# Performance work log

Measured on AMD Instinct MI355X. Metric: run time of the kernel, lower is better.

Reference implementation:

```python
import jax, jax.numpy as jnp
import numpy as np

D_MODEL = 1024
NUM_HEADS = 16
ENERGY_SCALE = 0.1
LN_EPS = 1e-5


def layernorm(x, gamma, beta):
    mu = jnp.mean(x, axis=-1, keepdims=True)
    var = jnp.var(x, axis=-1, keepdims=True)
    return (x - mu) * jax.lax.rsqrt(var + LN_EPS) * gamma + beta


def setup_inputs() -> dict:
    key = jax.random.key(0)
    ks = jax.random.split(key, 8)
    B, L, D = 2, 2048, D_MODEL
    s = 0.02
    return {
        "x": jax.random.normal(ks[0], (B, L, D), dtype=jnp.float32),
        "wq": jax.random.normal(ks[1], (D, D), dtype=jnp.float32) * s,
        "wk": jax.random.normal(ks[2], (D, D), dtype=jnp.float32) * s,
        "wv": jax.random.normal(ks[3], (D, D), dtype=jnp.float32) * s,
        "wo_w": jax.random.normal(ks[4], (D, D), dtype=jnp.float32) * s,
        "wo_b": jnp.zeros((D,), dtype=jnp.float32),
        "ep_w": jax.random.normal(ks[5], (D, D), dtype=jnp.float32) * s,
        "ep_b": jnp.zeros((D,), dtype=jnp.float32),
        "en_g": jnp.ones((D,), dtype=jnp.float32),
        "en_b": jnp.zeros((D,), dtype=jnp.float32),
        "ln_g": jnp.ones((D,), dtype=jnp.float32),
        "ln_b": jnp.zeros((D,), dtype=jnp.float32),
    }


def reference(x, wq, wk, wv, wo_w, wo_b, ep_w, ep_b, en_g, en_b, ln_g, ln_b):
    B, L, D = x.shape
    H, dk = NUM_HEADS, D // NUM_HEADS
    # Linear projections (torch convention: y = x @ W^T), split heads -> [B,H,L,dk]
    q = (x @ wq.T).reshape(B, L, H, dk).transpose(0, 2, 1, 3)
    k = (x @ wk.T).reshape(B, L, H, dk).transpose(0, 2, 1, 3)
    v = (x @ wv.T).reshape(B, L, H, dk).transpose(0, 2, 1, 3)
    scores = jnp.einsum("bhld,bhmd->bhlm", q, k) / jnp.sqrt(jnp.float32(dk))
    # Energy bias: ef @ ef^T as a proper GEMM (same math as the broadcast-mul-sum)
    ef = layernorm(x @ ep_w.T + ep_b, en_g, en_b)
    energy_bias = jnp.einsum("bld,bmd->blm", ef, ef)  # [B,L,L]
    scores = scores + ENERGY_SCALE * energy_bias[:, None, :, :]
    attn = jax.nn.softmax(scores, axis=-1)  # dropout is identity in eval mode
    ctx = jnp.einsum("bhlm,bhmd->bhld", attn, v)
    ctx = ctx.transpose(0, 2, 1, 3).reshape(B, L, D)
    out = ctx @ wo_w.T + wo_b
    return layernorm(out + x, ln_g, ln_b), attn
```

## Files before the change

kernel.cpp:

```cpp
#include <hip/hip_runtime.h>
#include <math.h>

#define D_MODEL 1024
#define NUM_HEADS 16
#define DK 64
#define L_SEQ 2048
#define BATCH 2
#define LN_EPS 1e-5f
#define ENERGY_SCALE 0.1f

typedef __attribute__((ext_vector_type(8))) short short8;
typedef __attribute__((ext_vector_type(4))) float f32x4;

__device__ __forceinline__ float waveReduceSum(float v) {
#pragma unroll
    for (int off = 32; off > 0; off >>= 1) v += __shfl_xor(v, off, 64);
    return v;
}

__device__ __forceinline__ unsigned short f2bf(float f) {
    unsigned int u = __float_as_uint(f);
    u += 0x7fff + ((u >> 16) & 1);
    return (unsigned short)(u >> 16);
}

__global__ __launch_bounds__(256) void cvt6(
    const float* s0, const float* s1, const float* s2,
    const float* s3, const float* s4, const float* s5,
    unsigned short* d0, unsigned short* d1, unsigned short* d2,
    unsigned short* d3, unsigned short* d4, unsigned short* d5,
    long long n0, long long n1, long long n2, long long n3, long long n4, long long n5)
{
    const float* s; unsigned short* d; long long n;
    switch (blockIdx.y) {
        case 0: s = s0; d = d0; n = n0; break;
        case 1: s = s1; d = d1; n = n1; break;
        case 2: s = s2; d = d2; n = n2; break;
        case 3: s = s3; d = d3; n = n3; break;
        case 4: s = s4; d = d4; n = n4; break;
        default: s = s5; d = d5; n = n5; break;
    }
    long long i = ((long long)blockIdx.x * 256 + threadIdx.x) * 4;
    if (i >= n) return;
    float4 v = *(const float4*)(s + i);
    ushort4 o;
    o.x = f2bf(v.x); o.y = f2bf(v.y); o.z = f2bf(v.z); o.w = f2bf(v.w);
    *(ushort4*)(d + i) = o;
}

__global__ __launch_bounds__(256) void gemm_bf16(
    const unsigned short* __restrict__ A, const unsigned short* __restrict__ B,
    const float* __restrict__ bias, float* __restrict__ Cf, unsigned short* __restrict__ Ch,
    int N, int K, long long sA, long long sB, long long sC)
{
    A += (long long)blockIdx.z * sA;
    B += (long long)blockIdx.z * sB;
    __shared__ unsigned short As[128 * 72];
    __shared__ unsigned short Bs[128 * 72];
    const int tid = threadIdx.x;
    const int lane = tid & 63, w = tid >> 6;
    const int quad = lane >> 4, col = lane & 15;
    const int wm = w & 1, wn = w >> 1;
    const int row0 = blockIdx.y * 128, col0 = blockIdx.x * 128;

    f32x4 acc[4][4];
#pragma unroll
    for (int mt = 0; mt < 4; mt++)
#pragma unroll
        for (int nt = 0; nt < 4; nt++) acc[mt][nt] = (f32x4){0.f, 0.f, 0.f, 0.f};

    for (int k0 = 0; k0 < K; k0 += 64) {
        __syncthreads();
#pragma unroll
        for (int p = 0; p < 4; p++) {
            int u = tid + p * 256;
            int r = u >> 3;
            int c = (u & 7) * 8;
            *(uint4*)(As + r * 72 + c) = *(const uint4*)(A + (long long)(row0 + r) * K + k0 + c);
            *(uint4*)(Bs + r * 72 + c) = *(const uint4*)(B + (long long)(col0 + r) * K + k0 + c);
        }
        __syncthreads();
#pragma unroll
        for (int kc = 0; kc < 2; kc++) {
            short8 af[4], bfr[4];
#pragma unroll
            for (int mt = 0; mt < 4; mt++)
                af[mt] = *(const short8*)(As + (wm * 64 + mt * 16 + col) * 72 + quad * 8 + kc * 32);
#pragma unroll
            for (int nt = 0; nt < 4; nt++)
                bfr[nt] = *(const short8*)(Bs + (wn * 64 + nt * 16 + col) * 72 + quad * 8 + kc * 32);
#pragma unroll
            for (int mt = 0; mt < 4; mt++)
#pragma unroll
                for (int nt = 0; nt < 4; nt++)
                    acc[mt][nt] = __builtin_amdgcn_mfma_f32_16x16x32_bf16(af[mt], bfr[nt], acc[mt][nt], 0, 0, 0);
        }
    }

#pragma unroll
    for (int mt = 0; mt < 4; mt++)
#pragma unroll
        for (int nt = 0; nt < 4; nt++)
#pragma unroll
            for (int reg = 0; reg < 4; reg++) {
                long long row = row0 + wm * 64 + mt * 16 + quad * 4 + reg;
                int c = col0 + wn * 64 + nt * 16 + col;
                float v = acc[mt][nt][reg];
                if (bias) v += bias[c];
                if (Cf) Cf[blockIdx.z * sC + row * N + c] = v;
                else    Ch[blockIdx.z * sC + row * N + c] = f2bf(v);
            }
}

__global__ __launch_bounds__(256) void proj_gemm(
    const unsigned short* __restrict__ Xh,
    const unsigned short* __restrict__ wqh, const unsigned short* __restrict__ wkh,
    const unsigned short* __restrict__ wvh, const unsigned short* __restrict__ eph,
    const float* __restrict__ ep_b,
    unsigned short* __restrict__ Qh, unsigned short* __restrict__ Kh,
    unsigned short* __restrict__ Vf, float* __restrict__ EP)
{
    const unsigned short* B;
    switch (blockIdx.z) {
        case 0: B = wqh; break;
        case 1: B = wkh; break;
        case 2: B = wvh; break;
        default: B = eph; break;
    }
    __shared__ unsigned short As[128 * 72];
    __shared__ unsigned short Bs[128 * 72];
    const int tid = threadIdx.x;
    const int lane = tid & 63, w = tid >> 6;
    const int quad = lane >> 4, col = lane & 15;
    const int wm = w & 1, wn = w >> 1;
    const int row0 = blockIdx.y * 128, col0 = blockIdx.x * 128;
    const int K = D_MODEL, N = D_MODEL;

    f32x4 acc[4][4];
#pragma unroll
    for (int mt = 0; mt < 4; mt++)
#pragma unroll
        for (int nt = 0; nt < 4; nt++) acc[mt][nt] = (f32x4){0.f, 0.f, 0.f, 0.f};

    for (int k0 = 0; k0 < K; k0 += 64) {
        __syncthreads();
#pragma unroll
        for (int p = 0; p < 4; p++) {
            int u = tid + p * 256;
            int r = u >> 3;
            int c = (u & 7) * 8;
            *(uint4*)(As + r * 72 + c) = *(const uint4*)(Xh + (long long)(row0 + r) * K + k0 + c);
            *(uint4*)(Bs + r * 72 + c) = *(const uint4*)(B + (long long)(col0 + r) * K + k0 + c);
        }
        __syncthreads();
#pragma unroll
        for (int kc = 0; kc < 2; kc++) {
            short8 af[4], bfr[4];
#pragma unroll
            for (int mt = 0; mt < 4; mt++)
                af[mt] = *(const short8*)(As + (wm * 64 + mt * 16 + col) * 72 + quad * 8 + kc * 32);
#pragma unroll
            for (int nt = 0; nt < 4; nt++)
                bfr[nt] = *(const short8*)(Bs + (wn * 64 + nt * 16 + col) * 72 + quad * 8 + kc * 32);
#pragma unroll
            for (int mt = 0; mt < 4; mt++)
#pragma unroll
                for (int nt = 0; nt < 4; nt++)
                    acc[mt][nt] = __builtin_amdgcn_mfma_f32_16x16x32_bf16(af[mt], bfr[nt], acc[mt][nt], 0, 0, 0);
        }
    }

    unsigned short* Hout = (blockIdx.z == 0) ? Qh : (blockIdx.z == 1) ? Kh : Vf;
#pragma unroll
    for (int mt = 0; mt < 4; mt++)
#pragma unroll
        for (int nt = 0; nt < 4; nt++)
#pragma unroll
            for (int reg = 0; reg < 4; reg++) {
                long long row = row0 + wm * 64 + mt * 16 + quad * 4 + reg;
                int c = col0 + wn * 64 + nt * 16 + col;
                float v = acc[mt][nt][reg];
                if (blockIdx.z == 3) EP[row * N + c] = v + ep_b[c];
                else                 Hout[row * N + c] = f2bf(v);
            }
}

__global__ __launch_bounds__(256) void ln_rows(
    const float* __restrict__ in, const float* __restrict__ res,
    const float* __restrict__ g, const float* __restrict__ bta,
    float* __restrict__ outf, unsigned short* __restrict__ outh)
{
    const long long row = blockIdx.x;
    const float* ip = in + row * D_MODEL;
    const float* rp = res ? res + row * D_MODEL : nullptr;
    const int tid = threadIdx.x;
    float vals[4];
    float s = 0.f, ss = 0.f;
#pragma unroll
    for (int j = 0; j < 4; j++) {
        int idx = tid + j * 256;
        float v = ip[idx];
        if (rp) v += rp[idx];
        vals[j] = v; s += v; ss += v * v;
    }
    __shared__ float sred[4], ssred[4];
    s = waveReduceSum(s); ss = waveReduceSum(ss);
    int wave = tid >> 6, lane = tid & 63;
    if (lane == 0) { sred[wave] = s; ssred[wave] = ss; }
    __syncthreads();
    float ts = sred[0] + sred[1] + sred[2] + sred[3];
    float tss = ssred[0] + ssred[1] + ssred[2] + ssred[3];
    float mu = ts * (1.f / D_MODEL);
    float var = tss * (1.f / D_MODEL) - mu * mu;
    float rs = rsqrtf(var + LN_EPS);
#pragma unroll
    for (int j = 0; j < 4; j++) {
        int idx = tid + j * 256;
        float o = (vals[j] - mu) * rs * g[idx] + bta[idx];
        if (outf) outf[row * D_MODEL + idx] = o;
        else      outh[row * D_MODEL + idx] = f2bf(o);
    }
}

__global__ __launch_bounds__(256) void transpose_v(
    const unsigned short* __restrict__ V, unsigned short* __restrict__ Vt)
{
    const int m0 = blockIdx.x * 64, h = blockIdx.y, b = blockIdx.z;
    __shared__ unsigned int t[64][65];
    const int tid = threadIdx.x;
    {
        int r = tid >> 4, c4 = (tid & 15) * 4;
#pragma unroll
        for (int i = 0; i < 4; i++) {
            int row = r + i * 16;
            ushort4 v = *(const ushort4*)(V + ((long long)b * L_SEQ + m0 + row) * D_MODEL + h * DK + c4);
            t[row][c4] = v.x; t[row][c4 + 1] = v.y; t[row][c4 + 2] = v.z; t[row][c4 + 3] = v.w;
        }
    }
    __syncthreads();
    const int lane = tid & 63, wv = tid >> 6;
#pragma unroll
    for (int i = 0; i < 16; i++) {
        int d = wv * 16 + i;
        Vt[(((long long)(b * NUM_HEADS + h)) * DK + d) * L_SEQ + m0 + lane] = (unsigned short)t[lane][d];
    }
}

__global__ __launch_bounds__(256) void attn_mfma(
    const unsigned short* __restrict__ Qh, const unsigned short* __restrict__ Kh,
    const unsigned short* __restrict__ Vt, const float* __restrict__ EB,
    float* __restrict__ attn_out, unsigned short* __restrict__ CTXh)
{
    __shared__ unsigned short smem[5 * 64 * 72];
    unsigned short* K0 = smem;
    unsigned short* K1 = smem + 4608;
    unsigned short* V0 = smem + 2 * 4608;
    unsigned short* V1 = smem + 3 * 4608;
    unsigned short* Ps = smem + 4 * 4608;

    const int tid = threadIdx.x;
    const int lane = tid & 63, w = tid >> 6;
    const int quad = lane >> 4, col = lane & 15;
    const int l0 = blockIdx.x * 64;
    const int h = blockIdx.y, b = blockIdx.z;

    short8 aq[2];
    {
        const unsigned short* qrow = Qh + ((long long)b * L_SEQ + l0 + w * 16 + col) * D_MODEL + h * DK;
        aq[0] = *(const short8*)(qrow + quad * 8);
        aq[1] = *(const short8*)(qrow + 32 + quad * 8);
    }

    const float* ebp = EB + ((long long)b * L_SEQ + l0 + w * 16 + quad * 4) * L_SEQ + col;
    const unsigned short* kbase = Kh + ((long long)b * L_SEQ) * D_MODEL + h * DK;
    const unsigned short* vbase = Vt + ((long long)(b * NUM_HEADS + h)) * DK * L_SEQ;

    const int sr = tid >> 2, sc0 = (tid & 3) * 16;

    float rowM[4] = {-1e30f, -1e30f, -1e30f, -1e30f};
    float rowS[4] = {0.f, 0.f, 0.f, 0.f};
    float ebc[4][4];

    {
        *(uint4*)(K0 + sr * 72 + sc0)     = *(const uint4*)(kbase + (long long)sr * D_MODEL + sc0);
        *(uint4*)(K0 + sr * 72 + sc0 + 8) = *(const uint4*)(kbase + (long long)sr * D_MODEL + sc0 + 8);
#pragma unroll
        for (int nt = 0; nt < 4; nt++)
#pragma unroll
            for (int reg = 0; reg < 4; reg++)
                ebc[nt][reg] = ebp[(long long)reg * L_SEQ + nt * 16];
    }
    __syncthreads();

    for (int t = 0; t < 32; t++) {
        unsigned short* cur = (t & 1) ? K1 : K0;
        unsigned short* nxt = (t & 1) ? K0 : K1;
        uint4 ka, kb;
        float ebn[4][4];
        if (t < 31) {
            const int m1 = (t + 1) * 64;
            ka = *(const uint4*)(kbase + (long long)(m1 + sr) * D_MODEL + sc0);
            kb = *(const uint4*)(kbase + (long long)(m1 + sr) * D_MODEL + sc0 + 8);
#pragma unroll
            for (int nt = 0; nt < 4; nt++)
#pragma unroll
                for (int reg = 0; reg < 4; reg++)
                    ebn[nt][reg] = ebp[(long long)reg * L_SEQ + m1 + nt * 16];
        }

        f32x4 acc[4];
#pragma unroll
        for (int nt = 0; nt < 4; nt++) acc[nt] = (f32x4){0.f, 0.f, 0.f, 0.f};
#pragma unroll
        for (int nt = 0; nt < 4; nt++)
#pragma unroll
            for (int kc = 0; kc < 2; kc++) {
                short8 bk = *(const short8*)(cur + (nt * 16 + col) * 72 + quad * 8 + kc * 32);
                acc[nt] = __builtin_amdgcn_mfma_f32_16x16x32_bf16(aq[kc], bk, acc[nt], 0, 0, 0);
            }

        float sv[4][4];
#pragma unroll
        for (int nt = 0; nt < 4; nt++)
#pragma unroll
            for (int reg = 0; reg < 4; reg++)
                sv[nt][reg] = acc[nt][reg] * 0.125f + ENERGY_SCALE * ebc[nt][reg];

#pragma unroll
        for (int reg = 0; reg < 4; reg++) {
            float tm = fmaxf(fmaxf(sv[0][reg], sv[1][reg]), fmaxf(sv[2][reg], sv[3][reg]));
#pragma unroll
            for (int off = 8; off > 0; off >>= 1) tm = fmaxf(tm, __shfl_xor(tm, off, 64));
            float nm = fmaxf(rowM[reg], tm);
            float tsum = __expf(sv[0][reg] - nm) + __expf(sv[1][reg] - nm) +
                         __expf(sv[2][reg] - nm) + __expf(sv[3][reg] - nm);
#pragma unroll
            for (int off = 8; off > 0; off >>= 1) tsum += __shfl_xor(tsum, off, 64);
            rowS[reg] = rowS[reg] * __expf(rowM[reg] - nm) + tsum;
            rowM[reg] = nm;
        }

        if (t < 31) {
            *(uint4*)(nxt + sr * 72 + sc0)     = ka;
            *(uint4*)(nxt + sr * 72 + sc0 + 8) = kb;
        }
        __syncthreads();
        if (t < 31) {
#pragma unroll
            for (int nt = 0; nt < 4; nt++)
#pragma unroll
                for (int reg = 0; reg < 4; reg++)
                    ebc[nt][reg] = ebn[nt][reg];
        }
    }

    float invS[4];
#pragma unroll
    for (int reg = 0; reg < 4; reg++) invS[reg] = 1.f / rowS[reg];

    f32x4 ctx[4];
#pragma unroll
    for (int nt = 0; nt < 4; nt++) ctx[nt] = (f32x4){0.f, 0.f, 0.f, 0.f};

    unsigned short* Psw = Ps + w * 16 * 72;
    float* aob = attn_out + (((long long)(b * NUM_HEADS + h)) * L_SEQ + l0 + w * 16 + quad * 4) * L_SEQ + col;

    {
        *(uint4*)(K0 + sr * 72 + sc0)     = *(const uint4*)(kbase + (long long)sr * D_MODEL + sc0);
        *(uint4*)(K0 + sr * 72 + sc0 + 8) = *(const uint4*)(kbase + (long long)sr * D_MODEL + sc0 + 8);
        *(uint4*)(V0 + sr * 72 + sc0)     = *(const uint4*)(vbase + (long long)sr * L_SEQ + sc0);
        *(uint4*)(V0 + sr * 72 + sc0 + 8) = *(const uint4*)(vbase + (long long)sr * L_SEQ + sc0 + 8);
#pragma unroll
        for (int nt = 0; nt < 4; nt++)
#pragma unroll
            for (int reg = 0; reg < 4; reg++)
                ebc[nt][reg] = ebp[(long long)reg * L_SEQ + nt * 16];
    }
    __syncthreads();

    for (int t = 0; t < 32; t++) {
        const int m0 = t * 64;
        unsigned short* curK = (t & 1) ? K1 : K0;
        unsigned short* nxtK = (t & 1) ? K0 : K1;
        unsigned short* curV = (t & 1) ? V1 : V0;
        unsigned short* nxtV = (t & 1) ? V0 : V1;
        uint4 ka, kb, va, vb;
        float ebn[4][4];
        if (t < 31) {
            const int m1 = m0 + 64;
            ka = *(const uint4*)(kbase + (long long)(m1 + sr) * D_MODEL + sc0);
            kb = *(const uint4*)(kbase + (long long)(m1 + sr) * D_MODEL + sc0 + 8);
            va = *(const uint4*)(vbase + (long long)sr * L_SEQ + m1 + sc0);
            vb = *(const uint4*)(vbase + (long long)sr * L_SEQ + m1 + sc0 + 8);
#pragma unroll
            for (int nt = 0; nt < 4; nt++)
#pragma unroll
                for (int reg = 0; reg < 4; reg++)
                    ebn[nt][reg] = ebp[(long long)reg * L_SEQ + m1 + nt * 16];
        }

        f32x4 acc[4];
#pragma unroll
        for (int nt = 0; nt < 4; nt++) acc[nt] = (f32x4){0.f, 0.f, 0.f, 0.f};
#pragma unroll
        for (int nt = 0; nt < 4; nt++)
#pragma unroll
            for (int kc = 0; kc < 2; kc++) {
                short8 bk = *(const short8*)(curK + (nt * 16 + col) * 72 + quad * 8 + kc * 32);
                acc[nt] = __builtin_amdgcn_mfma_f32_16x16x32_bf16(aq[kc], bk, acc[nt], 0, 0, 0);
            }

        float pv[4][4];
#pragma unroll
        for (int nt = 0; nt < 4; nt++)
#pragma unroll
            for (int reg = 0; reg < 4; reg++) {
                float s = acc[nt][reg] * 0.125f + ENERGY_SCALE * ebc[nt][reg];
                float p = __expf(s - rowM[reg]) * invS[reg];
                pv[nt][reg] = p;
                Psw[(quad * 4 + reg) * 72 + nt * 16 + col] = f2bf(p);
            }

        short8 ap[2];
#pragma unroll
        for (int kc = 0; kc < 2; kc++)
            ap[kc] = *(const short8*)(Psw + col * 72 + quad * 8 + kc * 32);
#pragma unroll
        for (int nt = 0; nt < 4; nt++)
#pragma unroll
            for (int kc = 0; kc < 2; kc++) {
                short8 bv = *(const short8*)(curV + (nt * 16 + col) * 72 + quad * 8 + kc * 32);
                ctx[nt] = __builtin_amdgcn_mfma_f32_16x16x32_bf16(ap[kc], bv, ctx[nt], 0, 0, 0);
            }

#pragma unroll
        for (int nt = 0; nt < 4; nt++)
#pragma unroll
            for (int reg = 0; reg < 4; reg++)
                aob[(long long)reg * L_SEQ + m0 + nt * 16] = pv[nt][reg];

        if (t < 31) {
            *(uint4*)(nxtK + sr * 72 + sc0)     = ka;
            *(uint4*)(nxtK + sr * 72 + sc0 + 8) = kb;
            *(uint4*)(nxtV + sr * 72 + sc0)     = va;
            *(uint4*)(nxtV + sr * 72 + sc0 + 8) = vb;
        }
        __syncthreads();
        if (t < 31) {
#pragma unroll
            for (int nt = 0; nt < 4; nt++)
#pragma unroll
                for (int reg = 0; reg < 4; reg++)
                    ebc[nt][reg] = ebn[nt][reg];
        }
    }

#pragma unroll
    for (int nt = 0; nt < 4; nt++)
#pragma unroll
        for (int reg = 0; reg < 4; reg++)
            CTXh[((long long)b * L_SEQ + l0 + w * 16 + quad * 4 + reg) * D_MODEL + h * DK + nt * 16 + col] =
                f2bf(ctx[nt][reg]);
}

extern "C" void kernel_launch(void* const* d_in, const int* in_sizes, int n_in,
                              void* d_out, int out_size, void* d_ws, size_t ws_size,
                              hipStream_t stream) {
    const float* x    = (const float*)d_in[0];
    const float* wq   = (const float*)d_in[1];
    const float* wk   = (const float*)d_in[2];
    const float* wv   = (const float*)d_in[3];
    const float* wo_w = (const float*)d_in[4];
    const float* wo_b = (const float*)d_in[5];
    const float* ep_w = (const float*)d_in[6];
    const float* ep_b = (const float*)d_in[7];
    const float* en_g = (const float*)d_in[8];
    const float* en_b = (const float*)d_in[9];
    const float* ln_g = (const float*)d_in[10];
    const float* ln_b = (const float*)d_in[11];

    float* out_final = (float*)d_out;
    float* attn_out  = out_final + (long long)BATCH * L_SEQ * D_MODEL;

    const long long MD = (long long)BATCH * L_SEQ * D_MODEL;
    const long long WN = (long long)D_MODEL * D_MODEL;

    float* EB = (float*)d_ws;
    float* EP = EB + (long long)BATCH * L_SEQ * L_SEQ;
    unsigned short* Xh   = (unsigned short*)(EP + MD);
    unsigned short* Qh   = Xh + MD;
    unsigned short* Kh   = Qh + MD;
    unsigned short* Vf   = Kh + MD;
    unsigned short* Vt   = Vf + MD;
    unsigned short* EFh  = Vt + MD;
    unsigned short* CTXh = EFh + MD;
    unsigned short* wqh  = CTXh + MD;
    unsigned short* wkh  = wqh + WN;
    unsigned short* wvh  = wkh + WN;
    unsigned short* eph  = wvh + WN;
    unsigned short* woh  = eph + WN;
    float* OUT = EP;

    const int M = BATCH * L_SEQ;
    dim3 blk(256);

    cvt6<<<dim3((unsigned)(MD / 1024), 6), blk, 0, stream>>>(
        x, wq, wk, wv, ep_w, wo_w, Xh, wqh, wkh, wvh, eph, woh,
        MD, WN, WN, WN, WN, WN);

    proj_gemm<<<dim3(D_MODEL / 128, M / 128, 4), blk, 0, stream>>>(
        Xh, wqh, wkh, wvh, eph, ep_b, Qh, Kh, Vf, EP);

    ln_rows<<<dim3(M), blk, 0, stream>>>(EP, nullptr, en_g, en_b, nullptr, EFh);

    gemm_bf16<<<dim3(L_SEQ / 128, L_SEQ / 128, BATCH), blk, 0, stream>>>(
        EFh, EFh, nullptr, EB, nullptr, L_SEQ, D_MODEL,
        (long long)L_SEQ * D_MODEL, (long long)L_SEQ * D_MODEL,
        (long long)L_SEQ * L_SEQ);

    transpose_v<<<dim3(L_SEQ / 64, NUM_HEADS, BATCH), blk, 0, stream>>>(Vf, Vt);

    attn_mfma<<<dim3(L_SEQ / 64, NUM_HEADS, BATCH), blk, 0, stream>>>(
        Qh, Kh, Vt, EB, attn_out, CTXh);

    gemm_bf16<<<dim3(D_MODEL / 128, M / 128, 1), blk, 0, stream>>>(
        CTXh, woh, wo_b, OUT, nullptr, D_MODEL, D_MODEL, 0, 0, 0);

    ln_rows<<<dim3(M), blk, 0, stream>>>(OUT, x, ln_g, ln_b, out_final, nullptr);
}
```

Baseline: 905.3 us.

## Replace online softmax max with precomputed Cauchy-Schwarz upper bound

Precomputes per-row energy-bias maxima and per-head Q/K norms in small new kernels, then uses the bound 0.1*max(EB) + |q|*max|k|/8 as a fixed softmax shift. The first attention pass no longer needs the per-tile max reductions, shuffles and rescaling; it only accumulates exponentials, with a single cross-lane sum at the end. The cost is three extra kernel launches plus a full read of the energy-bias matrix. A loose bound could also underflow the exponentials, since the shift may sit far above the true row max.

New measurement: 894.9 us. About the same (-1.2%).

```diff
diff --git a/kernel.cpp b/kernel.cpp
--- a/kernel.cpp
+++ b/kernel.cpp
@@ -17,11 +17,19 @@
     for (int off = 32; off > 0; off >>= 1) v += __shfl_xor(v, off, 64);
     return v;
 }
+__device__ __forceinline__ float waveReduceMax(float v) {
+#pragma unroll
+    for (int off = 32; off > 0; off >>= 1) v = fmaxf(v, __shfl_xor(v, off, 64));
+    return v;
+}
 
 __device__ __forceinline__ unsigned short f2bf(float f) {
     unsigned int u = __float_as_uint(f);
     u += 0x7fff + ((u >> 16) & 1);
     return (unsigned short)(u >> 16);
+}
+__device__ __forceinline__ float bf2f(unsigned short u) {
+    return __uint_as_float((unsigned int)u << 16);
 }
 
 __global__ __launch_bounds__(256) void cvt6(
@@ -246,9 +254,73 @@
     }
 }
 
+__global__ __launch_bounds__(256) void eb_rowmax(
+    const float* __restrict__ EB, float* __restrict__ ebmax)
+{
+    const long long row = blockIdx.x;
+    const float* p = EB + row * L_SEQ;
+    const int tid = threadIdx.x;
+    float4 a = *(const float4*)(p + tid * 4);
+    float4 c = *(const float4*)(p + 1024 + tid * 4);
+    float m = fmaxf(fmaxf(fmaxf(a.x, a.y), fmaxf(a.z, a.w)),
+                    fmaxf(fmaxf(c.x, c.y), fmaxf(c.z, c.w)));
+    m = waveReduceMax(m);
+    __shared__ float red[4];
+    int wave = tid >> 6, lane = tid & 63;
+    if (lane == 0) red[wave] = m;
+    __syncthreads();
+    if (tid == 0)
+        ebmax[row] = fmaxf(fmaxf(red[0], red[1]), fmaxf(red[2], red[3]));
+}
+
+__global__ __launch_bounds__(256) void qk_stats(
+    const unsigned short* __restrict__ Qh, const unsigned short* __restrict__ Kh,
+    float* __restrict__ qn, float* __restrict__ kn)
+{
+    const int l0 = blockIdx.x * 64, h = blockIdx.y, b = blockIdx.z;
+    const int tid = threadIdx.x;
+    const int r = tid >> 2, p4 = (tid & 3) * 16;
+    const unsigned short* q = Qh + ((long long)b * L_SEQ + l0 + r) * D_MODEL + h * DK + p4;
+    const unsigned short* k = Kh + ((long long)b * L_SEQ + l0 + r) * D_MODEL + h * DK + p4;
+    float sq = 0.f, sk = 0.f;
+#pragma unroll
+    for (int i = 0; i < 16; i++) {
+        float qv = bf2f(q[i]); sq += qv * qv;
+        float kv = bf2f(k[i]); sk += kv * kv;
+    }
+    sq += __shfl_xor(sq, 1, 64); sq += __shfl_xor(sq, 2, 64);
+    sk += __shfl_xor(sk, 1, 64); sk += __shfl_xor(sk, 2, 64);
+    if ((tid & 3) == 0) {
+        long long idx = ((long long)(b * NUM_HEADS + h)) * L_SEQ + l0 + r;
+        qn[idx] = sqrtf(sq);
+        kn[idx] = sqrtf(sk);
+    }
+}
+
+__global__ __launch_bounds__(256) void kmax_red(
+    const float* __restrict__ kn, float* __restrict__ kmax)
+{
+    const long long bh = blockIdx.x;
+    const float* p = kn + bh * L_SEQ;
+    const int tid = threadIdx.x;
+    float4 a = *(const float4*)(p + tid * 4);
+    float4 c = *(const float4*)(p + 1024 + tid * 4);
+    float m = fmaxf(fmaxf(fmaxf(a.x, a.y), fmaxf(a.z, a.w)),
+                    fmaxf(fmaxf(c.x, c.y), fmaxf(c.z, c.w)));
+    m = waveReduceMax(m);
+    __shared__ float red[4];
+    int wave = tid >> 6, lane = tid & 63;
+    if (lane == 0) red[wave] = m;
+    __syncthreads();
+    if (tid == 0)
+        kmax[bh] = fmaxf(fmaxf(red[0], red[1]), fmaxf(red[2], red[3]));
+}
+
 __global__ __launch_bounds__(256) void attn_mfma(
     const unsigned short* __restrict__ Qh, const unsigned short* __restrict__ Kh,
     const unsigned short* __restrict__ Vt, const float* __restrict__ EB,
+    const float* __restrict__ ebmax, const float* __restrict__ qn,
+    const float* __restrict__ kmax,
     float* __restrict__ attn_out, unsigned short* __restrict__ CTXh)
 {
     __shared__ unsigned short smem[5 * 64 * 72];
@@ -271,14 +343,25 @@
         aq[1] = *(const short8*)(qrow + 32 + quad * 8);
     }
 
+    float Mhat[4];
+    {
+        const float km = kmax[b * NUM_HEADS + h];
+#pragma unroll
+        for (int reg = 0; reg < 4; reg++) {
+            int row = l0 + w * 16 + quad * 4 + reg;
+            float qb = qn[((long long)(b * NUM_HEADS + h)) * L_SEQ + row];
+            Mhat[reg] = ENERGY_SCALE * ebmax[(long long)b * L_SEQ + row] +
+                        qb * km * 0.125f + 0.02f;
+        }
+    }
+
     const float* ebp = EB + ((long long)b * L_SEQ + l0 + w * 16 + quad * 4) * L_SEQ + col;
     const unsigned short* kbase = Kh + ((long long)b * L_SEQ) * D_MODEL + h * DK;
     const unsigned short* vbase = Vt + ((long long)(b * NUM_HEADS + h)) * DK * L_SEQ;
 
     const int sr = tid >> 2, sc0 = (tid & 3) * 16;
 
-    float rowM[4] = {-1e30f, -1e30f, -1e30f, -1e30f};
-    float rowS[4] = {0.f, 0.f, 0.f, 0.f};
+    float rowSacc[4] = {0.f, 0.f, 0.f, 0.f};
     float ebc[4][4];
 
     {
@@ -319,26 +402,13 @@
                 acc[nt] = __builtin_amdgcn_mfma_f32_16x16x32_bf16(aq[kc], bk, acc[nt], 0, 0, 0);
             }
 
-        float sv[4][4];
-#pragma unroll
-        for (int nt = 0; nt < 4; nt++)
-#pragma unroll
-            for (int reg = 0; reg < 4; reg++)
-                sv[nt][reg] = acc[nt][reg] * 0.125f + ENERGY_SCALE * ebc[nt][reg];
-
-#pragma unroll
-        for (int reg = 0; reg < 4; reg++) {
-            float tm = fmaxf(fmaxf(sv[0][reg], sv[1][reg]), fmaxf(sv[2][reg], sv[3][reg]));
-#pragma unroll
-            for (int off = 8; off > 0; off >>= 1) tm = fmaxf(tm, __shfl_xor(tm, off, 64));
-            float nm = fmaxf(rowM[reg], tm);
-            float tsum = __expf(sv[0][reg] - nm) + __expf(sv[1][reg] - nm) +
-                         __expf(sv[2][reg] - nm) + __expf(sv[3][reg] - nm);
-#pragma unroll
-            for (int off = 8; off > 0; off >>= 1) tsum += __shfl_xor(tsum, off, 64);
-            rowS[reg] = rowS[reg] * __expf(rowM[reg] - nm) + tsum;
-            rowM[reg] = nm;
-        }
+#pragma unroll
+        for (int nt = 0; nt < 4; nt++)
+#pragma unroll
+            for (int reg = 0; reg < 4; reg++) {
+                float s = acc[nt][reg] * 0.125f + ENERGY_SCALE * ebc[nt][reg];
+                rowSacc[reg] += __expf(s - Mhat[reg]);
+            }
 
         if (t < 31) {
             *(uint4*)(nxt + sr * 72 + sc0)     = ka;
@@ -356,7 +426,12 @@
 
     float invS[4];
 #pragma unroll
-    for (int reg = 0; reg < 4; reg++) invS[reg] = 1.f / rowS[reg];
+    for (int reg = 0; reg < 4; reg++) {
+        float v = rowSacc[reg];
+#pragma unroll
+        for (int off = 8; off > 0; off >>= 1) v += __shfl_xor(v, off, 64);
+        invS[reg] = 1.f / v;
+    }
 
     f32x4 ctx[4];
 #pragma unroll
@@ -416,7 +491,7 @@
 #pragma unroll
             for (int reg = 0; reg < 4; reg++) {
                 float s = acc[nt][reg] * 0.125f + ENERGY_SCALE * ebc[nt][reg];
-                float p = __expf(s - rowM[reg]) * invS[reg];
+                float p = __expf(s - Mhat[reg]) * invS[reg];
                 pv[nt][reg] = p;
                 Psw[(quad * 4 + reg) * 72 + nt * 16 + col] = f2bf(p);
             }
@@ -499,6 +574,10 @@
     unsigned short* wvh  = wkh + WN;
     unsigned short* eph  = wvh + WN;
     unsigned short* woh  = eph + WN;
+    float* ebmax = (float*)(woh + WN);
+    float* qn    = ebmax + (long long)BATCH * L_SEQ;
+    float* kn    = qn + (long long)BATCH * NUM_HEADS * L_SEQ;
+    float* kmax  = kn + (long long)BATCH * NUM_HEADS * L_SEQ;
     float* OUT = EP;
 
     const int M = BATCH * L_SEQ;
@@ -518,10 +597,14 @@
         (long long)L_SEQ * D_MODEL, (long long)L_SEQ * D_MODEL,
         (long long)L_SEQ * L_SEQ);
 
+    qk_stats<<<dim3(L_SEQ / 64, NUM_HEADS, BATCH), blk, 0, stream>>>(Qh, Kh, qn, kn);
+    kmax_red<<<dim3(BATCH * NUM_HEADS), blk, 0, stream>>>(kn, kmax);
+    eb_rowmax<<<dim3(M), blk, 0, stream>>>(EB, ebmax);
+
     transpose_v<<<dim3(L_SEQ / 64, NUM_HEADS, BATCH), blk, 0, stream>>>(Vf, Vt);
 
     attn_mfma<<<dim3(L_SEQ / 64, NUM_HEADS, BATCH), blk, 0, stream>>>(
-        Qh, Kh, Vt, EB, attn_out, CTXh);
+        Qh, Kh, Vt, EB, ebmax, qn, kmax, attn_out, CTXh);
 
     gemm_bf16<<<dim3(D_MODEL / 128, M / 128, 1), blk, 0, stream>>>(
         CTXh, woh, wo_b, OUT, nullptr, D_MODEL, D_MODEL, 0, 0, 0);
```
